# Kernel optimization log

Hardware: AMD Instinct MI355X
Metric: run time of the kernel (lower is better)

Reference implementation:

```python
import jax, jax.numpy as jnp
import numpy as np

DIM = 2048
N_HEADS = 32
N_KV_HEADS = 8
HEAD_DIM = DIM // N_HEADS  # 64
GROUP = N_HEADS // N_KV_HEADS  # 4
ROPE_BASE = 10000.0


def setup_inputs() -> dict:
    key = jax.random.key(0)
    k1, k2, k3, k4, k5 = jax.random.split(key, 5)
    b, s = 1, 2048
    scale = 1.0 / np.sqrt(DIM)
    return {
        "x": jax.random.normal(k1, (b, s, DIM), dtype=jnp.float32),
        # weights stored as (in, out); equivalent math to torch Linear (x @ W.T)
        "wq": jax.random.normal(k2, (DIM, N_HEADS * HEAD_DIM), dtype=jnp.float32) * scale,
        "wk": jax.random.normal(k3, (DIM, N_KV_HEADS * HEAD_DIM), dtype=jnp.float32) * scale,
        "wv": jax.random.normal(k4, (DIM, N_KV_HEADS * HEAD_DIM), dtype=jnp.float32) * scale,
        "wo": jax.random.normal(k5, (N_HEADS * HEAD_DIM, DIM), dtype=jnp.float32) * scale,
    }


def _rope_cos_sin(seq_len, dtype):
    inv_freq = 1.0 / (ROPE_BASE ** (jnp.arange(0, HEAD_DIM, 2, dtype=jnp.float32) / HEAD_DIM))
    t = jnp.arange(seq_len, dtype=jnp.float32)
    freqs = jnp.outer(t, inv_freq)              # [s, hd/2]
    emb = jnp.concatenate([freqs, freqs], -1)   # [s, hd]
    return jnp.cos(emb).astype(dtype), jnp.sin(emb).astype(dtype)


def _rotate_half(x):
    x1, x2 = x[..., : HEAD_DIM // 2], x[..., HEAD_DIM // 2 :]
    return jnp.concatenate([-x2, x1], axis=-1)


def reference(x, wq, wk, wv, wo):
    b, s, _ = x.shape
    q = (x @ wq).reshape(b, s, N_HEADS, HEAD_DIM)
    k = (x @ wk).reshape(b, s, N_KV_HEADS, HEAD_DIM)
    v = (x @ wv).reshape(b, s, N_KV_HEADS, HEAD_DIM)

    cos, sin = _rope_cos_sin(s, x.dtype)
    cos = cos[None, :, None, :]  # [1, s, 1, hd] broadcast over batch & heads
    sin = sin[None, :, None, :]
    q = q * cos + _rotate_half(q) * sin
    k = k * cos + _rotate_half(k) * sin

    # GQA: repeat KV heads (repeat_interleave along head dim)
    k = jnp.repeat(k, GROUP, axis=2)  # [b, s, n_heads, hd]
    v = jnp.repeat(v, GROUP, axis=2)

    q = q.transpose(0, 2, 1, 3)  # [b, h, s, d]
    k = k.transpose(0, 2, 1, 3)
    v = v.transpose(0, 2, 1, 3)

    scores = jnp.einsum("bhqd,bhkd->bhqk", q, k) / jnp.sqrt(jnp.asarray(HEAD_DIM, x.dtype))
    attn = jax.nn.softmax(scores, axis=-1)
    out = jnp.einsum("bhqk,bhkd->bhqd", attn, v)
    out = out.transpose(0, 2, 1, 3).reshape(b, s, N_HEADS * HEAD_DIM)
    return out @ wo
```

## Files before the change

### kernel.cpp

```cpp
#include <hip/hip_runtime.h>
#include <hip/hip_bf16.h>

typedef __bf16 bf16x8 __attribute__((ext_vector_type(8)));
typedef __bf16 bf16x4 __attribute__((ext_vector_type(4)));
typedef float fx4 __attribute__((ext_vector_type(4)));
typedef float fx16 __attribute__((ext_vector_type(16)));

#define AS1 __attribute__((address_space(1)))
#define AS3 __attribute__((address_space(3)))

__global__ __launch_bounds__(256) void cast_x(const float4* __restrict__ X, __bf16* __restrict__ Xb) {
    int i = blockIdx.x * 256 + threadIdx.x;
    float4 v = X[i];
    bf16x4 o = { (__bf16)v.x, (__bf16)v.y, (__bf16)v.z, (__bf16)v.w };
    *(bf16x4*)(Xb + (size_t)i * 4) = o;
}

__global__ __launch_bounds__(256) void transpose_all(const float* __restrict__ wq, const float* __restrict__ wk,
                                                     const float* __restrict__ wv, const float* __restrict__ wo,
                                                     __bf16* __restrict__ WqkvT, __bf16* __restrict__ WoT) {
    constexpr int K = 2048;
    __shared__ float t[32][33];
    const int bx = blockIdx.x;
    const float* W; __bf16* Wt; int N, n0;
    if (bx < 64)      { W = wq; Wt = WqkvT;                        N = 2048; n0 = bx * 32; }
    else if (bx < 80) { W = wk; Wt = WqkvT + (size_t)2048 * 2048;  N = 512;  n0 = (bx - 64) * 32; }
    else if (bx < 96) { W = wv; Wt = WqkvT + (size_t)2560 * 2048;  N = 512;  n0 = (bx - 80) * 32; }
    else              { W = wo; Wt = WoT;                          N = 2048; n0 = (bx - 96) * 32; }
    const int tx = threadIdx.x & 31, ty = threadIdx.x >> 5;
    const int k0 = blockIdx.y * 32;
#pragma unroll
    for (int i = 0; i < 4; ++i)
        t[ty + i * 8][tx] = W[(size_t)(k0 + ty + i * 8) * N + n0 + tx];
    __syncthreads();
#pragma unroll
    for (int i = 0; i < 4; ++i)
        Wt[(size_t)(n0 + ty + i * 8) * K + k0 + tx] = (__bf16)t[tx][ty + i * 8];
}

__global__ __launch_bounds__(256) void gemm_qkv(const __bf16* __restrict__ A, const __bf16* __restrict__ Bt,
                                                __bf16* __restrict__ Qr, __bf16* __restrict__ Kr,
                                                __bf16* __restrict__ Vt) {
    constexpr int K = 2048;
    __shared__ __align__(16) __bf16 lA[128 * 32];
    __shared__ __align__(16) __bf16 lB[64 * 32];
    const int tid = threadIdx.x;
    const int wave = tid >> 6, lane = tid & 63;
    const int quad = lane >> 4, l16 = lane & 15;
    const int m0 = blockIdx.x * 128, n0 = blockIdx.y * 64;
    fx4 acc[2][4] = {};

    int cr[3], cc[3];
    const __bf16* csrc[3];
    __bf16* cdst[3];
#pragma unroll
    for (int it = 0; it < 3; ++it) {
        const int c = wave * 3 + it;
        if (c < 8) {
            const int boff = c * 1024 + lane * 16;
            cr[it] = boff >> 6; cc[it] = (boff & 63) >> 1;
            csrc[it] = A + (size_t)(m0 + cr[it]) * K;
            cdst[it] = lA + c * 512;
        } else {
            const int boff = (c - 8) * 1024 + lane * 16;
            cr[it] = boff >> 6; cc[it] = (boff & 63) >> 1;
            csrc[it] = Bt + (size_t)(n0 + cr[it]) * K;
            cdst[it] = lB + (c - 8) * 512;
        }
    }

    for (int k0 = 0; k0 < K; k0 += 32) {
        __syncthreads();
#pragma unroll
        for (int it = 0; it < 3; ++it)
            __builtin_amdgcn_global_load_lds((const AS1 void*)(csrc[it] + k0 + cc[it]),
                                             (AS3 void*)cdst[it], 16, 0, 0);
        __builtin_amdgcn_s_waitcnt(0);
        __syncthreads();

        bf16x8 af[2], bfr[4];
#pragma unroll
        for (int i = 0; i < 2; ++i) af[i] = *(const bf16x8*)&lA[(wave * 32 + i * 16 + l16) * 32 + quad * 8];
#pragma unroll
        for (int j = 0; j < 4; ++j) bfr[j] = *(const bf16x8*)&lB[(j * 16 + l16) * 32 + quad * 8];
#pragma unroll
        for (int i = 0; i < 2; ++i)
#pragma unroll
            for (int j = 0; j < 4; ++j)
                acc[i][j] = __builtin_amdgcn_mfma_f32_16x16x32_bf16(af[i], bfr[j], acc[i][j], 0, 0, 0);
    }

    const int by = blockIdx.y;
    if (by < 40) {
        const float scale = (by < 32) ? 0.18033688011112042f : 1.0f;
        __bf16* base = (by < 32) ? (Qr + (size_t)by * 2048 * 64)
                                 : (Kr + (size_t)(by - 32) * 2048 * 64);
#pragma unroll
        for (int jj = 0; jj < 2; ++jj) {
            const int dlo = jj * 16 + l16;
            const float inv = __builtin_amdgcn_exp2f(-(float)dlo * 0.41524101186092029f);
#pragma unroll
            for (int i = 0; i < 2; ++i)
#pragma unroll
                for (int r = 0; r < 4; ++r) {
                    const int s = m0 + wave * 32 + i * 16 + quad * 4 + r;
                    float sn, cs;
                    __sincosf((float)s * inv, &sn, &cs);
                    const float lo = acc[i][jj][r], hv = acc[i][jj + 2][r];
                    base[(size_t)s * 64 + dlo]      = (__bf16)((lo * cs - hv * sn) * scale);
                    base[(size_t)s * 64 + dlo + 32] = (__bf16)((hv * cs + lo * sn) * scale);
                }
        }
    } else {
        __bf16* vb = Vt + (size_t)(by - 40) * 64 * 2048;
#pragma unroll
        for (int i = 0; i < 2; ++i)
#pragma unroll
            for (int j = 0; j < 4; ++j) {
                const int d = j * 16 + l16;
                const int s0 = m0 + wave * 32 + i * 16 + quad * 4;
                bf16x4 p;
#pragma unroll
                for (int r = 0; r < 4; ++r) p[r] = (__bf16)acc[i][j][r];
                *(bf16x4*)&vb[(size_t)d * 2048 + s0] = p;
            }
    }
}

__global__ __launch_bounds__(256) void gemm_bt_sk(const __bf16* __restrict__ A, const __bf16* __restrict__ Bt,
                                                  float* __restrict__ C0, float* __restrict__ C1,
                                                  int M, int N, int K) {
    __shared__ __align__(16) __bf16 lA[128 * 32];
    __shared__ __align__(16) __bf16 lB[128 * 32];
    const int tid = threadIdx.x;
    const int wave = tid >> 6, lane = tid & 63;
    const int quad = lane >> 4, l16 = lane & 15;
    const int m0 = blockIdx.x * 128, n0 = blockIdx.y * 128;
    const int kz = blockIdx.z;
    const int kbeg = kz * (K >> 1), kend = kbeg + (K >> 1);
    float* C = kz ? C1 : C0;
    const int wm = (wave >> 1) * 64, wn = (wave & 1) * 64;
    fx4 acc[4][4] = {};

    const int st0 = wave * 1024;
    const int st1 = 4096 + wave * 1024;
    const int r0 = (st0 + lane * 16) >> 6, c0 = ((st0 + lane * 16) & 63) >> 1;
    const int r1 = (st1 + lane * 16) >> 6, c1 = ((st1 + lane * 16) & 63) >> 1;

    for (int k0 = kbeg; k0 < kend; k0 += 32) {
        __syncthreads();
        __builtin_amdgcn_global_load_lds((const AS1 void*)(A + (size_t)(m0 + r0) * K + k0 + c0),
                                         (AS3 void*)(lA + (st0 >> 1)), 16, 0, 0);
        __builtin_amdgcn_global_load_lds((const AS1 void*)(A + (size_t)(m0 + r1) * K + k0 + c1),
                                         (AS3 void*)(lA + (st1 >> 1)), 16, 0, 0);
        __builtin_amdgcn_global_load_lds((const AS1 void*)(Bt + (size_t)(n0 + r0) * K + k0 + c0),
                                         (AS3 void*)(lB + (st0 >> 1)), 16, 0, 0);
        __builtin_amdgcn_global_load_lds((const AS1 void*)(Bt + (size_t)(n0 + r1) * K + k0 + c1),
                                         (AS3 void*)(lB + (st1 >> 1)), 16, 0, 0);
        __builtin_amdgcn_s_waitcnt(0);
        __syncthreads();

        bf16x8 af[4], bfr[4];
#pragma unroll
        for (int i = 0; i < 4; ++i) af[i] = *(const bf16x8*)&lA[(wm + i * 16 + l16) * 32 + quad * 8];
#pragma unroll
        for (int j = 0; j < 4; ++j) bfr[j] = *(const bf16x8*)&lB[(wn + j * 16 + l16) * 32 + quad * 8];
#pragma unroll
        for (int i = 0; i < 4; ++i)
#pragma unroll
            for (int j = 0; j < 4; ++j)
                acc[i][j] = __builtin_amdgcn_mfma_f32_16x16x32_bf16(af[i], bfr[j], acc[i][j], 0, 0, 0);
    }
#pragma unroll
    for (int i = 0; i < 4; ++i)
#pragma unroll
        for (int j = 0; j < 4; ++j) {
            const int row = m0 + wm + i * 16 + quad * 4;
            const int col = n0 + wn + j * 16 + l16;
#pragma unroll
            for (int r = 0; r < 4; ++r)
                C[(size_t)(row + r) * N + col] = acc[i][j][r];
        }
}

__global__ __launch_bounds__(256) void reduce_add(float4* __restrict__ out, const float4* __restrict__ p) {
    const int i = blockIdx.x * 256 + threadIdx.x;
    float4 a = out[i];
    const float4 b = p[i];
    a.x += b.x; a.y += b.y; a.z += b.z; a.w += b.w;
    out[i] = a;
}

__global__ __launch_bounds__(256, 2) void flash_attn(const __bf16* __restrict__ Qr, const __bf16* __restrict__ Kr,
                                                     const __bf16* __restrict__ Vt, __bf16* __restrict__ O) {
    constexpr int S = 2048;
    __shared__ __align__(16) __bf16 lK[64 * 72];
    __shared__ __align__(16) __bf16 lV[64 * 72];
    __shared__ __align__(16) __bf16 lP[4][32 * 72];
    const int qt = blockIdx.x, h = blockIdx.y, kvh = h >> 2;
    const int tid = threadIdx.x, wave = tid >> 6, lane = tid & 63;
    const int l32 = lane & 31, hi = lane >> 5;

    const int qrow = qt * 128 + wave * 32 + l32;
    const __bf16* qptr = Qr + ((size_t)h * S + qrow) * 64;
    bf16x8 qf[4];
#pragma unroll
    for (int kc = 0; kc < 4; ++kc) qf[kc] = *(const bf16x8*)(qptr + kc * 16 + hi * 8);

    const __bf16* Kbase = Kr + (size_t)kvh * S * 64;
    const __bf16* Vbase = Vt + (size_t)kvh * 64 * S;

    const int krow = tid >> 3;
    const int kcol = (tid & 7) * 8;

    bf16x8 kreg0 = *(const bf16x8*)(Kbase + (size_t)krow * 64 + kcol);
    bf16x8 kreg1 = *(const bf16x8*)(Kbase + (size_t)(32 + krow) * 64 + kcol);
    bf16x8 vreg0 = *(const bf16x8*)(Vbase + (size_t)krow * S + kcol);
    bf16x8 vreg1 = *(const bf16x8*)(Vbase + (size_t)(32 + krow) * S + kcol);

    fx16 ov0, ov1;
#pragma unroll
    for (int i = 0; i < 16; ++i) { ov0[i] = 0.f; ov1[i] = 0.f; }
    float l_acc = 0.f;
    __bf16* lPw = &lP[wave][0];

    for (int kt = 0; kt < S / 64; ++kt) {
        __syncthreads();
        *(bf16x8*)&lK[krow * 72 + kcol] = kreg0;
        *(bf16x8*)&lK[(32 + krow) * 72 + kcol] = kreg1;
        *(bf16x8*)&lV[krow * 72 + kcol] = vreg0;
        *(bf16x8*)&lV[(32 + krow) * 72 + kcol] = vreg1;
        const int ktn = (kt + 1 < S / 64) ? kt + 1 : kt;
        kreg0 = *(const bf16x8*)(Kbase + (size_t)(ktn * 64 + krow) * 64 + kcol);
        kreg1 = *(const bf16x8*)(Kbase + (size_t)(ktn * 64 + 32 + krow) * 64 + kcol);
        vreg0 = *(const bf16x8*)(Vbase + (size_t)krow * S + ktn * 64 + kcol);
        vreg1 = *(const bf16x8*)(Vbase + (size_t)(32 + krow) * S + ktn * 64 + kcol);
        __syncthreads();

        fx16 sc0, sc1;
#pragma unroll
        for (int i = 0; i < 16; ++i) { sc0[i] = 0.f; sc1[i] = 0.f; }
#pragma unroll
        for (int kc = 0; kc < 4; ++kc) {
            const bf16x8 a0 = *(const bf16x8*)&lK[l32 * 72 + kc * 16 + hi * 8];
            const bf16x8 a1 = *(const bf16x8*)&lK[(32 + l32) * 72 + kc * 16 + hi * 8];
            sc0 = __builtin_amdgcn_mfma_f32_32x32x16_bf16(a0, qf[kc], sc0, 0, 0, 0);
            sc1 = __builtin_amdgcn_mfma_f32_32x32x16_bf16(a1, qf[kc], sc1, 0, 0, 0);
        }

#pragma unroll
        for (int mt = 0; mt < 2; ++mt) {
#pragma unroll
            for (int rg2 = 0; rg2 < 4; ++rg2) {
                bf16x4 pk;
#pragma unroll
                for (int r = 0; r < 4; ++r) {
                    const float p = __builtin_amdgcn_exp2f(mt ? sc1[rg2 * 4 + r] : sc0[rg2 * 4 + r]);
                    l_acc += p;
                    pk[r] = (__bf16)p;
                }
                *(bf16x4*)&lPw[l32 * 72 + mt * 32 + rg2 * 8 + hi * 4] = pk;
            }
        }

#pragma unroll
        for (int kc = 0; kc < 4; ++kc) {
            const bf16x8 pb = *(const bf16x8*)&lPw[l32 * 72 + kc * 16 + hi * 8];
            const bf16x8 va0 = *(const bf16x8*)&lV[l32 * 72 + kc * 16 + hi * 8];
            const bf16x8 va1 = *(const bf16x8*)&lV[(32 + l32) * 72 + kc * 16 + hi * 8];
            ov0 = __builtin_amdgcn_mfma_f32_32x32x16_bf16(va0, pb, ov0, 0, 0, 0);
            ov1 = __builtin_amdgcn_mfma_f32_32x32x16_bf16(va1, pb, ov1, 0, 0, 0);
        }
    }

    const float l_tot = l_acc + __shfl_xor(l_acc, 32, 64);
    const float inv_l = 1.0f / l_tot;

#pragma unroll
    for (int dt = 0; dt < 2; ++dt)
#pragma unroll
        for (int rg2 = 0; rg2 < 4; ++rg2) {
            bf16x4 o4;
#pragma unroll
            for (int r = 0; r < 4; ++r)
                o4[r] = (__bf16)((dt ? ov1[rg2 * 4 + r] : ov0[rg2 * 4 + r]) * inv_l);
            const int col = h * 64 + dt * 32 + rg2 * 8 + hi * 4;
            *(bf16x4*)(O + (size_t)qrow * 2048 + col) = o4;
        }
}

extern "C" void kernel_launch(void* const* d_in, const int* in_sizes, int n_in,
                              void* d_out, int out_size, void* d_ws, size_t ws_size,
                              hipStream_t stream) {
    const float* x  = (const float*)d_in[0];
    const float* wq = (const float*)d_in[1];
    const float* wk = (const float*)d_in[2];
    const float* wv = (const float*)d_in[3];
    const float* wo = (const float*)d_in[4];
    float* out = (float*)d_out;
    char* ws = (char*)d_ws;

    __bf16* Xb    = (__bf16*)ws;
    __bf16* WqkvT = (__bf16*)(ws + ((size_t)8 << 20));
    __bf16* WoT   = (__bf16*)(ws + ((size_t)20 << 20));
    __bf16* Qr    = (__bf16*)(ws + ((size_t)28 << 20));
    __bf16* Kr    = (__bf16*)(ws + ((size_t)36 << 20));
    __bf16* Vt    = (__bf16*)(ws + ((size_t)38 << 20));
    __bf16* Ob    = (__bf16*)(ws + ((size_t)40 << 20));
    float*  Cp    = (float*)ws;

    cast_x<<<4096, 256, 0, stream>>>((const float4*)x, Xb);
    transpose_all<<<dim3(160, 64), 256, 0, stream>>>(wq, wk, wv, wo, WqkvT, WoT);

    gemm_qkv<<<dim3(16, 48), 256, 0, stream>>>(Xb, WqkvT, Qr, Kr, Vt);
    flash_attn<<<dim3(16, 32), 256, 0, stream>>>(Qr, Kr, Vt, Ob);
    gemm_bt_sk<<<dim3(16, 16, 2), 256, 0, stream>>>(Ob, WoT, out, Cp, 2048, 2048, 2048);
    reduce_add<<<4096, 256, 0, stream>>>((float4*)out, (const float4*)Cp);
}
```

Before: 231.0 us.

## Split KV sequence across two wave groups in flash attention and reduce in LDS

Doubles the flash attention block to 512 threads, with two groups of four waves each handling alternating 64-key tiles for the same 128 query rows. Partial outputs and row sums from the second group are passed through LDS and added by the first group before normalization. The aim is more waves per CU and more latency hiding on the 512-block grid, at the cost of extra LDS, a final reduction step, and tighter register limits from the launch bounds.

Result: no change. 232.1 us (+0.5%).

```diff
diff --git a/kernel.cpp b/kernel.cpp
--- a/kernel.cpp
+++ b/kernel.cpp
@@ -191,17 +191,18 @@
     out[i] = a;
 }
 
-__global__ __launch_bounds__(256, 2) void flash_attn(const __bf16* __restrict__ Qr, const __bf16* __restrict__ Kr,
+__global__ __launch_bounds__(512, 4) void flash_attn(const __bf16* __restrict__ Qr, const __bf16* __restrict__ Kr,
                                                      const __bf16* __restrict__ Vt, __bf16* __restrict__ O) {
     constexpr int S = 2048;
-    __shared__ __align__(16) __bf16 lK[64 * 72];
-    __shared__ __align__(16) __bf16 lV[64 * 72];
-    __shared__ __align__(16) __bf16 lP[4][32 * 72];
+    __shared__ __align__(16) __bf16 lK[2][64 * 72];
+    __shared__ __align__(16) __bf16 lV[2][64 * 72];
+    __shared__ __align__(16) __bf16 lP[8][32 * 72];
     const int qt = blockIdx.x, h = blockIdx.y, kvh = h >> 2;
     const int tid = threadIdx.x, wave = tid >> 6, lane = tid & 63;
+    const int grp = wave >> 2, w4 = wave & 3;
     const int l32 = lane & 31, hi = lane >> 5;
 
-    const int qrow = qt * 128 + wave * 32 + l32;
+    const int qrow = qt * 128 + w4 * 32 + l32;
     const __bf16* qptr = Qr + ((size_t)h * S + qrow) * 64;
     bf16x8 qf[4];
 #pragma unroll
@@ -210,27 +211,31 @@
     const __bf16* Kbase = Kr + (size_t)kvh * S * 64;
     const __bf16* Vbase = Vt + (size_t)kvh * 64 * S;
 
-    const int krow = tid >> 3;
-    const int kcol = (tid & 7) * 8;
-
-    bf16x8 kreg0 = *(const bf16x8*)(Kbase + (size_t)krow * 64 + kcol);
-    bf16x8 kreg1 = *(const bf16x8*)(Kbase + (size_t)(32 + krow) * 64 + kcol);
-    bf16x8 vreg0 = *(const bf16x8*)(Vbase + (size_t)krow * S + kcol);
-    bf16x8 vreg1 = *(const bf16x8*)(Vbase + (size_t)(32 + krow) * S + kcol);
+    const int gtid = tid & 255;
+    const int krow = gtid >> 3;
+    const int kcol = (gtid & 7) * 8;
+
+    bf16x8 kreg0 = *(const bf16x8*)(Kbase + (size_t)(grp * 64 + krow) * 64 + kcol);
+    bf16x8 kreg1 = *(const bf16x8*)(Kbase + (size_t)(grp * 64 + 32 + krow) * 64 + kcol);
+    bf16x8 vreg0 = *(const bf16x8*)(Vbase + (size_t)krow * S + grp * 64 + kcol);
+    bf16x8 vreg1 = *(const bf16x8*)(Vbase + (size_t)(32 + krow) * S + grp * 64 + kcol);
 
     fx16 ov0, ov1;
 #pragma unroll
     for (int i = 0; i < 16; ++i) { ov0[i] = 0.f; ov1[i] = 0.f; }
     float l_acc = 0.f;
     __bf16* lPw = &lP[wave][0];
-
-    for (int kt = 0; kt < S / 64; ++kt) {
-        __syncthreads();
-        *(bf16x8*)&lK[krow * 72 + kcol] = kreg0;
-        *(bf16x8*)&lK[(32 + krow) * 72 + kcol] = kreg1;
-        *(bf16x8*)&lV[krow * 72 + kcol] = vreg0;
-        *(bf16x8*)&lV[(32 + krow) * 72 + kcol] = vreg1;
-        const int ktn = (kt + 1 < S / 64) ? kt + 1 : kt;
+    __bf16* lKg = &lK[grp][0];
+    __bf16* lVg = &lV[grp][0];
+
+    for (int it = 0; it < 16; ++it) {
+        const int kt = it * 2 + grp;
+        __syncthreads();
+        *(bf16x8*)&lKg[krow * 72 + kcol] = kreg0;
+        *(bf16x8*)&lKg[(32 + krow) * 72 + kcol] = kreg1;
+        *(bf16x8*)&lVg[krow * 72 + kcol] = vreg0;
+        *(bf16x8*)&lVg[(32 + krow) * 72 + kcol] = vreg1;
+        const int ktn = (it + 1 < 16) ? kt + 2 : kt;
         kreg0 = *(const bf16x8*)(Kbase + (size_t)(ktn * 64 + krow) * 64 + kcol);
         kreg1 = *(const bf16x8*)(Kbase + (size_t)(ktn * 64 + 32 + krow) * 64 + kcol);
         vreg0 = *(const bf16x8*)(Vbase + (size_t)krow * S + ktn * 64 + kcol);
@@ -242,8 +247,8 @@
         for (int i = 0; i < 16; ++i) { sc0[i] = 0.f; sc1[i] = 0.f; }
 #pragma unroll
         for (int kc = 0; kc < 4; ++kc) {
-            const bf16x8 a0 = *(const bf16x8*)&lK[l32 * 72 + kc * 16 + hi * 8];
-            const bf16x8 a1 = *(const bf16x8*)&lK[(32 + l32) * 72 + kc * 16 + hi * 8];
+            const bf16x8 a0 = *(const bf16x8*)&lKg[l32 * 72 + kc * 16 + hi * 8];
+            const bf16x8 a1 = *(const bf16x8*)&lKg[(32 + l32) * 72 + kc * 16 + hi * 8];
             sc0 = __builtin_amdgcn_mfma_f32_32x32x16_bf16(a0, qf[kc], sc0, 0, 0, 0);
             sc1 = __builtin_amdgcn_mfma_f32_32x32x16_bf16(a1, qf[kc], sc1, 0, 0, 0);
         }
@@ -266,27 +271,51 @@
 #pragma unroll
         for (int kc = 0; kc < 4; ++kc) {
             const bf16x8 pb = *(const bf16x8*)&lPw[l32 * 72 + kc * 16 + hi * 8];
-            const bf16x8 va0 = *(const bf16x8*)&lV[l32 * 72 + kc * 16 + hi * 8];
-            const bf16x8 va1 = *(const bf16x8*)&lV[(32 + l32) * 72 + kc * 16 + hi * 8];
+            const bf16x8 va0 = *(const bf16x8*)&lVg[l32 * 72 + kc * 16 + hi * 8];
+            const bf16x8 va1 = *(const bf16x8*)&lVg[(32 + l32) * 72 + kc * 16 + hi * 8];
             ov0 = __builtin_amdgcn_mfma_f32_32x32x16_bf16(va0, pb, ov0, 0, 0, 0);
             ov1 = __builtin_amdgcn_mfma_f32_32x32x16_bf16(va1, pb, ov1, 0, 0, 0);
         }
     }
 
-    const float l_tot = l_acc + __shfl_xor(l_acc, 32, 64);
-    const float inv_l = 1.0f / l_tot;
-
-#pragma unroll
-    for (int dt = 0; dt < 2; ++dt)
-#pragma unroll
-        for (int rg2 = 0; rg2 < 4; ++rg2) {
-            bf16x4 o4;
-#pragma unroll
-            for (int r = 0; r < 4; ++r)
-                o4[r] = (__bf16)((dt ? ov1[rg2 * 4 + r] : ov0[rg2 * 4 + r]) * inv_l);
-            const int col = h * 64 + dt * 32 + rg2 * 8 + hi * 4;
-            *(bf16x4*)(O + (size_t)qrow * 2048 + col) = o4;
-        }
+    const float l_pair = l_acc + __shfl_xor(l_acc, 32, 64);
+
+    fx4* lO = (fx4*)&lP[0][0];
+    float* lL = (float*)&lK[0][0];
+    __syncthreads();
+    if (grp == 1) {
+#pragma unroll
+        for (int ic = 0; ic < 4; ++ic) {
+            fx4 c0, c1;
+#pragma unroll
+            for (int r = 0; r < 4; ++r) { c0[r] = ov0[ic * 4 + r]; c1[r] = ov1[ic * 4 + r]; }
+            lO[(ic * 4 + w4) * 64 + lane] = c0;
+            lO[((ic + 4) * 4 + w4) * 64 + lane] = c1;
+        }
+        if (hi == 0) lL[w4 * 32 + l32] = l_pair;
+    }
+    __syncthreads();
+    if (grp == 0) {
+#pragma unroll
+        for (int ic = 0; ic < 4; ++ic) {
+            const fx4 c0 = lO[(ic * 4 + w4) * 64 + lane];
+            const fx4 c1 = lO[((ic + 4) * 4 + w4) * 64 + lane];
+#pragma unroll
+            for (int r = 0; r < 4; ++r) { ov0[ic * 4 + r] += c0[r]; ov1[ic * 4 + r] += c1[r]; }
+        }
+        const float inv_l = 1.0f / (l_pair + lL[w4 * 32 + l32]);
+#pragma unroll
+        for (int dt = 0; dt < 2; ++dt)
+#pragma unroll
+            for (int rg2 = 0; rg2 < 4; ++rg2) {
+                bf16x4 o4;
+#pragma unroll
+                for (int r = 0; r < 4; ++r)
+                    o4[r] = (__bf16)((dt ? ov1[rg2 * 4 + r] : ov0[rg2 * 4 + r]) * inv_l);
+                const int col = h * 64 + dt * 32 + rg2 * 8 + hi * 4;
+                *(bf16x4*)(O + (size_t)qrow * 2048 + col) = o4;
+            }
+    }
 }
 
 extern "C" void kernel_launch(void* const* d_in, const int* in_sizes, int n_in,
@@ -313,7 +342,7 @@
     transpose_all<<<dim3(160, 64), 256, 0, stream>>>(wq, wk, wv, wo, WqkvT, WoT);
 
     gemm_qkv<<<dim3(16, 48), 256, 0, stream>>>(Xb, WqkvT, Qr, Kr, Vt);
-    flash_attn<<<dim3(16, 32), 256, 0, stream>>>(Qr, Kr, Vt, Ob);
+    flash_attn<<<dim3(16, 32), 512, 0, stream>>>(Qr, Kr, Vt, Ob);
     gemm_bt_sk<<<dim3(16, 16, 2), 256, 0, stream>>>(Ob, WoT, out, Cp, 2048, 2048, 2048);
     reduce_add<<<4096, 256, 0, stream>>>((float4*)out, (const float4*)Cp);
 }
```

## Feed attention P from registers via permuted V layout; widen QKV GEMM k-step

Applied to the files above, without the earlier changes.

In flash attention, the P tile is no longer written to and reread from shared memory. V columns are stored in a permuted order in LDS so the score accumulator registers can be packed straight into the B operand of the PV MFMA. Dropping the P buffer shrinks LDS use, and the launch bound is raised to allow more blocks per CU. The QKV GEMM now loads a 64-wide K slab per iteration into two LDS halves, halving the number of barrier/wait rounds at the cost of more LDS.

Result: no change. 228.0 us (-1.3%).

```diff
diff --git a/kernel.cpp b/kernel.cpp
--- a/kernel.cpp
+++ b/kernel.cpp
@@ -42,52 +42,52 @@
                                                 __bf16* __restrict__ Qr, __bf16* __restrict__ Kr,
                                                 __bf16* __restrict__ Vt) {
     constexpr int K = 2048;
-    __shared__ __align__(16) __bf16 lA[128 * 32];
-    __shared__ __align__(16) __bf16 lB[64 * 32];
+    __shared__ __align__(16) __bf16 lA[2][128 * 32];
+    __shared__ __align__(16) __bf16 lB[2][64 * 32];
     const int tid = threadIdx.x;
     const int wave = tid >> 6, lane = tid & 63;
     const int quad = lane >> 4, l16 = lane & 15;
     const int m0 = blockIdx.x * 128, n0 = blockIdx.y * 64;
     fx4 acc[2][4] = {};
 
-    int cr[3], cc[3];
-    const __bf16* csrc[3];
-    __bf16* cdst[3];
-#pragma unroll
-    for (int it = 0; it < 3; ++it) {
-        const int c = wave * 3 + it;
-        if (c < 8) {
-            const int boff = c * 1024 + lane * 16;
-            cr[it] = boff >> 6; cc[it] = (boff & 63) >> 1;
-            csrc[it] = A + (size_t)(m0 + cr[it]) * K;
-            cdst[it] = lA + c * 512;
+    const __bf16* csrc[6]; __bf16* cdst[6];
+#pragma unroll
+    for (int it = 0; it < 6; ++it) {
+        const int idx = wave * 6 + it;
+        const int r4 = lane >> 2, c8 = (lane & 3) * 8;
+        if (idx < 16) {
+            const int kh = idx & 1, s = idx >> 1;
+            csrc[it] = A + (size_t)(m0 + s * 16 + r4) * K + kh * 32 + c8;
+            cdst[it] = &lA[kh][s * 512 + lane * 8];
         } else {
-            const int boff = (c - 8) * 1024 + lane * 16;
-            cr[it] = boff >> 6; cc[it] = (boff & 63) >> 1;
-            csrc[it] = Bt + (size_t)(n0 + cr[it]) * K;
-            cdst[it] = lB + (c - 8) * 512;
-        }
-    }
-
-    for (int k0 = 0; k0 < K; k0 += 32) {
-        __syncthreads();
-#pragma unroll
-        for (int it = 0; it < 3; ++it)
-            __builtin_amdgcn_global_load_lds((const AS1 void*)(csrc[it] + k0 + cc[it]),
+            const int b = idx - 16, kh = b & 1, s = b >> 1;
+            csrc[it] = Bt + (size_t)(n0 + s * 16 + r4) * K + kh * 32 + c8;
+            cdst[it] = &lB[kh][s * 512 + lane * 8];
+        }
+    }
+
+    for (int k0 = 0; k0 < K; k0 += 64) {
+        __syncthreads();
+#pragma unroll
+        for (int it = 0; it < 6; ++it)
+            __builtin_amdgcn_global_load_lds((const AS1 void*)(csrc[it] + k0),
                                              (AS3 void*)cdst[it], 16, 0, 0);
         __builtin_amdgcn_s_waitcnt(0);
         __syncthreads();
 
-        bf16x8 af[2], bfr[4];
-#pragma unroll
-        for (int i = 0; i < 2; ++i) af[i] = *(const bf16x8*)&lA[(wave * 32 + i * 16 + l16) * 32 + quad * 8];
-#pragma unroll
-        for (int j = 0; j < 4; ++j) bfr[j] = *(const bf16x8*)&lB[(j * 16 + l16) * 32 + quad * 8];
-#pragma unroll
-        for (int i = 0; i < 2; ++i)
-#pragma unroll
-            for (int j = 0; j < 4; ++j)
-                acc[i][j] = __builtin_amdgcn_mfma_f32_16x16x32_bf16(af[i], bfr[j], acc[i][j], 0, 0, 0);
+#pragma unroll
+        for (int kc = 0; kc < 2; ++kc) {
+            bf16x8 af[2], bfr[4];
+#pragma unroll
+            for (int i = 0; i < 2; ++i) af[i] = *(const bf16x8*)&lA[kc][(wave * 32 + i * 16 + l16) * 32 + quad * 8];
+#pragma unroll
+            for (int j = 0; j < 4; ++j) bfr[j] = *(const bf16x8*)&lB[kc][(j * 16 + l16) * 32 + quad * 8];
+#pragma unroll
+            for (int i = 0; i < 2; ++i)
+#pragma unroll
+                for (int j = 0; j < 4; ++j)
+                    acc[i][j] = __builtin_amdgcn_mfma_f32_16x16x32_bf16(af[i], bfr[j], acc[i][j], 0, 0, 0);
+        }
     }
 
     const int by = blockIdx.y;
@@ -191,12 +191,11 @@
     out[i] = a;
 }
 
-__global__ __launch_bounds__(256, 2) void flash_attn(const __bf16* __restrict__ Qr, const __bf16* __restrict__ Kr,
+__global__ __launch_bounds__(256, 4) void flash_attn(const __bf16* __restrict__ Qr, const __bf16* __restrict__ Kr,
                                                      const __bf16* __restrict__ Vt, __bf16* __restrict__ O) {
     constexpr int S = 2048;
     __shared__ __align__(16) __bf16 lK[64 * 72];
     __shared__ __align__(16) __bf16 lV[64 * 72];
-    __shared__ __align__(16) __bf16 lP[4][32 * 72];
     const int qt = blockIdx.x, h = blockIdx.y, kvh = h >> 2;
     const int tid = threadIdx.x, wave = tid >> 6, lane = tid & 63;
     const int l32 = lane & 31, hi = lane >> 5;
@@ -212,6 +211,7 @@
 
     const int krow = tid >> 3;
     const int kcol = (tid & 7) * 8;
+    const int vslot = (kcol & 48) | ((kcol & 8) >> 1);
 
     bf16x8 kreg0 = *(const bf16x8*)(Kbase + (size_t)krow * 64 + kcol);
     bf16x8 kreg1 = *(const bf16x8*)(Kbase + (size_t)(32 + krow) * 64 + kcol);
@@ -222,15 +222,20 @@
 #pragma unroll
     for (int i = 0; i < 16; ++i) { ov0[i] = 0.f; ov1[i] = 0.f; }
     float l_acc = 0.f;
-    __bf16* lPw = &lP[wave][0];
-
-    for (int kt = 0; kt < S / 64; ++kt) {
+
+    for (int kt = 0; kt < 32; ++kt) {
         __syncthreads();
         *(bf16x8*)&lK[krow * 72 + kcol] = kreg0;
         *(bf16x8*)&lK[(32 + krow) * 72 + kcol] = kreg1;
-        *(bf16x8*)&lV[krow * 72 + kcol] = vreg0;
-        *(bf16x8*)&lV[(32 + krow) * 72 + kcol] = vreg1;
-        const int ktn = (kt + 1 < S / 64) ? kt + 1 : kt;
+        bf16x4 v0lo = { vreg0[0], vreg0[1], vreg0[2], vreg0[3] };
+        bf16x4 v0hi = { vreg0[4], vreg0[5], vreg0[6], vreg0[7] };
+        bf16x4 v1lo = { vreg1[0], vreg1[1], vreg1[2], vreg1[3] };
+        bf16x4 v1hi = { vreg1[4], vreg1[5], vreg1[6], vreg1[7] };
+        *(bf16x4*)&lV[krow * 72 + vslot]            = v0lo;
+        *(bf16x4*)&lV[krow * 72 + vslot + 8]        = v0hi;
+        *(bf16x4*)&lV[(32 + krow) * 72 + vslot]     = v1lo;
+        *(bf16x4*)&lV[(32 + krow) * 72 + vslot + 8] = v1hi;
+        const int ktn = (kt + 1 < 32) ? kt + 1 : kt;
         kreg0 = *(const bf16x8*)(Kbase + (size_t)(ktn * 64 + krow) * 64 + kcol);
         kreg1 = *(const bf16x8*)(Kbase + (size_t)(ktn * 64 + 32 + krow) * 64 + kcol);
         vreg0 = *(const bf16x8*)(Vbase + (size_t)krow * S + ktn * 64 + kcol);
@@ -249,27 +254,23 @@
         }
 
 #pragma unroll
-        for (int mt = 0; mt < 2; ++mt) {
-#pragma unroll
-            for (int rg2 = 0; rg2 < 4; ++rg2) {
-                bf16x4 pk;
-#pragma unroll
-                for (int r = 0; r < 4; ++r) {
-                    const float p = __builtin_amdgcn_exp2f(mt ? sc1[rg2 * 4 + r] : sc0[rg2 * 4 + r]);
+        for (int h2 = 0; h2 < 2; ++h2) {
+#pragma unroll
+            for (int c = 0; c < 2; ++c) {
+                bf16x8 pb;
+#pragma unroll
+                for (int j = 0; j < 8; ++j) {
+                    const float sv = h2 ? sc1[c * 8 + j] : sc0[c * 8 + j];
+                    const float p = __builtin_amdgcn_exp2f(sv);
                     l_acc += p;
-                    pk[r] = (__bf16)p;
+                    pb[j] = (__bf16)p;
                 }
-                *(bf16x4*)&lPw[l32 * 72 + mt * 32 + rg2 * 8 + hi * 4] = pk;
+                const int kcv = h2 * 2 + c;
+                const bf16x8 va0 = *(const bf16x8*)&lV[l32 * 72 + kcv * 16 + hi * 8];
+                const bf16x8 va1 = *(const bf16x8*)&lV[(32 + l32) * 72 + kcv * 16 + hi * 8];
+                ov0 = __builtin_amdgcn_mfma_f32_32x32x16_bf16(va0, pb, ov0, 0, 0, 0);
+                ov1 = __builtin_amdgcn_mfma_f32_32x32x16_bf16(va1, pb, ov1, 0, 0, 0);
             }
-        }
-
-#pragma unroll
-        for (int kc = 0; kc < 4; ++kc) {
-            const bf16x8 pb = *(const bf16x8*)&lPw[l32 * 72 + kc * 16 + hi * 8];
-            const bf16x8 va0 = *(const bf16x8*)&lV[l32 * 72 + kc * 16 + hi * 8];
-            const bf16x8 va1 = *(const bf16x8*)&lV[(32 + l32) * 72 + kc * 16 + hi * 8];
-            ov0 = __builtin_amdgcn_mfma_f32_32x32x16_bf16(va0, pb, ov0, 0, 0, 0);
-            ov1 = __builtin_amdgcn_mfma_f32_32x32x16_bf16(va1, pb, ov1, 0, 0, 0);
         }
     }
 
```
